# Performance work log

Measured on AMD Instinct MI355X. Metric: run time of the kernel, lower is better.

## Reference

```python
import jax, jax.numpy as jnp
import numpy as np

N = 50000
E = 800000
D = 512
H = 256
K = 16
COLLAPSE_REG = 1.0


def setup_inputs() -> dict:
    key = jax.random.key(0)
    ks = jax.random.split(key, 8)
    embeddings = jax.random.normal(ks[0], (N, D), dtype=jnp.float32)
    edge_src = jax.random.randint(ks[1], (E,), 0, N, dtype=jnp.int32)
    edge_dst = jax.random.randint(ks[2], (E,), 0, N, dtype=jnp.int32)
    # GCNConv params (glorot-ish scaling)
    W1 = jax.random.normal(ks[3], (D, H), dtype=jnp.float32) / np.sqrt(D)
    b1 = jnp.zeros((H,), dtype=jnp.float32)
    W2 = jax.random.normal(ks[4], (H, H), dtype=jnp.float32) / np.sqrt(H)
    b2 = jnp.zeros((H,), dtype=jnp.float32)
    Wa = jax.random.normal(ks[5], (H, K), dtype=jnp.float32) / np.sqrt(H)
    ba = jnp.zeros((K,), dtype=jnp.float32)
    return {"embeddings": embeddings, "edge_src": edge_src, "edge_dst": edge_dst,
            "W1": W1, "b1": b1, "W2": W2, "b2": b2, "Wa": Wa, "ba": ba}


def _gcn_conv(x, W, b, src, dst, dis):
    # PyG GCNConv: transform then D^{-1/2}(A+I)D^{-1/2} aggregation + bias.
    x = x @ W                                   # [N, out]
    norm = dis[src] * dis[dst]                  # [E]
    agg = jax.ops.segment_sum(x[src] * norm[:, None], dst, num_segments=N)
    agg = agg + (dis * dis)[:, None] * x        # self-loop term
    return agg + b


def reference(embeddings, edge_src, edge_dst, W1, b1, W2, b2, Wa, ba):
    # symmetric-norm degrees with self-loops (edge weight 1)
    deg = 1.0 + jax.ops.segment_sum(jnp.ones((E,), jnp.float32), edge_dst, num_segments=N)
    dis = jax.lax.rsqrt(deg)                    # deg > 0 always (self-loop)

    x = jax.nn.selu(_gcn_conv(embeddings, W1, b1, edge_src, edge_dst, dis))
    x_skip = x  # dropout is identity in eval
    x = jax.nn.selu(_gcn_conv(x, W2, b2, edge_src, edge_dst, dis))
    x = x + x_skip
    assignments = jax.nn.softmax(x @ Wa + ba, axis=1)   # [N, K]

    # ---- DMoN losses (faithful to original, incl. scalar normalizer) ----
    degrees = jax.ops.segment_sum(jnp.ones((E,), jnp.float32), edge_src, num_segments=N)  # row sums of A
    m = degrees.sum() / 2.0
    AS = jax.ops.segment_sum(assignments[edge_dst], edge_src, num_segments=N)  # A @ S, [N, K]
    trace_pooled = jnp.sum(assignments * AS)    # trace(S^T A S)
    dS = degrees @ assignments                  # [K]
    normalizer = jnp.dot(dS, dS) / (2.0 * m)    # scalar (as in original code)
    spectral_loss = -(trace_pooled - K * normalizer) / (2.0 * m)

    cluster_sizes = assignments.sum(axis=0)     # [K]
    collapse_loss = jnp.linalg.norm(cluster_sizes) / N * jnp.sqrt(jnp.float32(K)) - 1.0
    entropy = -jnp.sum(assignments * jnp.log(assignments + 1e-8)) / N
    entropy_loss = -0.1 * entropy
    total_loss = spectral_loss + COLLAPSE_REG * collapse_loss + entropy_loss

    pooled = (assignments / (cluster_sizes + 1e-8)).T @ embeddings  # [K, D]
    return (assignments, pooled, spectral_loss, COLLAPSE_REG * collapse_loss, total_loss, entropy_loss)
```

## Files before the change

### kernel.cpp

```cpp
#include <hip/hip_runtime.h>
#include <hip/hip_fp16.h>
#include <math.h>

#define NN 50000
#define EE 800000
#define DD 512
#define HH 256
#define KK 16
#define NB_SCAN 196

typedef _Float16 half8_t __attribute__((ext_vector_type(8)));
typedef float f32x4 __attribute__((ext_vector_type(4)));

__global__ void zero_kernel(int* __restrict__ p, int n) {
    int i = blockIdx.x * blockDim.x + threadIdx.x;
    if (i < n) p[i] = 0;
}

__global__ void count_kernel(const int4* __restrict__ src4, const int4* __restrict__ dst4,
                             int* __restrict__ indeg, int* __restrict__ outdeg) {
    int e = blockIdx.x * blockDim.x + threadIdx.x;
    if (e < EE / 4) {
        int4 s = src4[e], d = dst4[e];
        atomicAdd(&outdeg[s.x], 1); atomicAdd(&outdeg[s.y], 1);
        atomicAdd(&outdeg[s.z], 1); atomicAdd(&outdeg[s.w], 1);
        atomicAdd(&indeg[d.x], 1);  atomicAdd(&indeg[d.y], 1);
        atomicAdd(&indeg[d.z], 1);  atomicAdd(&indeg[d.w], 1);
    }
}

__global__ void scan_p1(const int* __restrict__ in, int* __restrict__ part, int n,
                        const int* __restrict__ outdeg, float* __restrict__ dis,
                        float* __restrict__ degf) {
    __shared__ int tile[256];
    int t = threadIdx.x;
    int i = blockIdx.x * 256 + t;
    int v = (i < n) ? in[i] : 0;
    tile[t] = v;
    if (i < n) {
        dis[i]  = 1.0f / sqrtf(1.0f + (float)v);
        degf[i] = (float)outdeg[i];
    }
    __syncthreads();
    for (int o = 128; o > 0; o >>= 1) {
        if (t < o) tile[t] += tile[t + o];
        __syncthreads();
    }
    if (t == 0) part[blockIdx.x] = tile[0];
}

__global__ void scan_p2(int* __restrict__ part, int nb, int* __restrict__ off_end) {
    __shared__ int tile[256];
    int t = threadIdx.x;
    int v = (t < nb) ? part[t] : 0;
    tile[t] = v;
    __syncthreads();
    for (int o = 1; o < 256; o <<= 1) {
        int x = (t >= o) ? tile[t - o] : 0;
        __syncthreads();
        tile[t] += x;
        __syncthreads();
    }
    if (t < nb) part[t] = tile[t] - v;
    if (t == 255) *off_end = tile[255];
}

__global__ void scan_p3(const int* __restrict__ in, const int* __restrict__ part,
                        int* __restrict__ out, int n) {
    __shared__ int tile[256];
    int t = threadIdx.x;
    int i = blockIdx.x * 256 + t;
    int v = (i < n) ? in[i] : 0;
    tile[t] = v;
    __syncthreads();
    for (int o = 1; o < 256; o <<= 1) {
        int x = (t >= o) ? tile[t - o] : 0;
        __syncthreads();
        tile[t] += x;
        __syncthreads();
    }
    if (i < n) out[i] = part[blockIdx.x] + tile[t] - v;
}

__global__ void scatter_kernel(const int4* __restrict__ src4, const int4* __restrict__ dst4,
                               const int* __restrict__ off, int* __restrict__ cur,
                               const float* __restrict__ dis,
                               int* __restrict__ nbr, __half* __restrict__ wgt) {
    int e = blockIdx.x * blockDim.x + threadIdx.x;
    if (e < EE / 4) {
        int4 s = src4[e], d = dst4[e];
        int p, q;
        p = atomicAdd(&cur[d.x], 1); q = off[d.x] + p;
        nbr[q] = s.x; wgt[q] = __float2half(dis[s.x] * dis[d.x]);
        p = atomicAdd(&cur[d.y], 1); q = off[d.y] + p;
        nbr[q] = s.y; wgt[q] = __float2half(dis[s.y] * dis[d.y]);
        p = atomicAdd(&cur[d.z], 1); q = off[d.z] + p;
        nbr[q] = s.z; wgt[q] = __float2half(dis[s.z] * dis[d.z]);
        p = atomicAdd(&cur[d.w], 1); q = off[d.w] + p;
        nbr[q] = s.w; wgt[q] = __float2half(dis[s.w] * dis[d.w]);
    }
}

__global__ void transpose_w(const float* __restrict__ W1, __half* __restrict__ Wt1,
                            const float* __restrict__ W2, __half* __restrict__ Wt2,
                            const float* __restrict__ Wa, __half* __restrict__ WaT) {
    int i = blockIdx.x * 256 + threadIdx.x;
    if (i < DD * HH) {
        int k = i / HH, n = i % HH;
        Wt1[(size_t)n * DD + k] = __float2half(W1[i]);
    } else if (i < DD * HH + HH * HH) {
        int j = i - DD * HH;
        int k = j / HH, n = j % HH;
        Wt2[(size_t)n * HH + k] = __float2half(W2[j]);
    } else if (i < DD * HH + HH * HH + HH * KK) {
        int j = i - DD * HH - HH * HH;
        int k = j / KK, n = j % KK;
        WaT[n * HH + k] = __float2half(Wa[j]);
    }
}

template <typename TA, int KDIM>
__global__ __launch_bounds__(256) void mfma_gemm(const TA* __restrict__ A,
                                                 const __half* __restrict__ Bt,
                                                 __half* __restrict__ C, int M) {
    constexpr bool F32 = sizeof(TA) == 4;
    constexpr int SROW = F32 ? 36 : 40;
    constexpr int EPG  = F32 ? 4 : 8;
    constexpr int GPR  = 32 / EPG;
    constexpr int RPP  = 256 / GPR;
    constexpr int NP   = 128 / RPP;
    constexpr int KI   = KDIM / 32;

    __shared__ TA As[2][128 * SROW];

    int t = threadIdx.x;
    int wave = t >> 6, lane = t & 63, quad = lane >> 4, l16 = lane & 15;
    int row0 = blockIdx.x * 128, col0 = blockIdx.y * 128;
    int wm = (wave & 1) * 64, wn = (wave >> 1) * 64;
    int srow = t / GPR, sg = t % GPR;

    f32x4 acc[4][4] = {};
    uint4 sreg[NP];
    uint4 bcur[4];

    const __half* brow[4];
#pragma unroll
    for (int ni = 0; ni < 4; ni++)
        brow[ni] = Bt + (size_t)(col0 + wn + ni * 16 + l16) * KDIM + quad * 8;

    auto gloadA = [&](int k0) {
#pragma unroll
        for (int p = 0; p < NP; p++) {
            int gr = row0 + p * RPP + srow;
            if (gr < M)
                sreg[p] = *(const uint4*)(A + (size_t)gr * KDIM + k0 + sg * EPG);
            else
                sreg[p] = make_uint4(0, 0, 0, 0);
        }
    };
    auto sstore = [&](int buf) {
#pragma unroll
        for (int p = 0; p < NP; p++)
            *(uint4*)&As[buf][(p * RPP + srow) * SROW + sg * EPG] = sreg[p];
    };

    gloadA(0);
#pragma unroll
    for (int ni = 0; ni < 4; ni++) bcur[ni] = *(const uint4*)(brow[ni]);
    sstore(0);
    __syncthreads();

#pragma unroll
    for (int i = 0; i < KI; i++) {
        int cur = i & 1;
        uint4 bnext[4];
        if (i + 1 < KI) {
            gloadA((i + 1) * 32);
#pragma unroll
            for (int ni = 0; ni < 4; ni++)
                bnext[ni] = *(const uint4*)(brow[ni] + (i + 1) * 32);
        }

        half8_t af[4];
#pragma unroll
        for (int mi = 0; mi < 4; mi++) {
            int row = wm + mi * 16 + l16;
            if constexpr (F32) {
                const float* pl = (const float*)&As[cur][0] + row * SROW + quad * 8;
                float4 x0 = *(const float4*)pl;
                float4 x1 = *(const float4*)(pl + 4);
                half8_t h;
                h[0] = (_Float16)x0.x; h[1] = (_Float16)x0.y;
                h[2] = (_Float16)x0.z; h[3] = (_Float16)x0.w;
                h[4] = (_Float16)x1.x; h[5] = (_Float16)x1.y;
                h[6] = (_Float16)x1.z; h[7] = (_Float16)x1.w;
                af[mi] = h;
            } else {
                af[mi] = *(const half8_t*)&As[cur][row * SROW + quad * 8];
            }
        }
#pragma unroll
        for (int mi = 0; mi < 4; mi++)
#pragma unroll
            for (int ni = 0; ni < 4; ni++)
                acc[mi][ni] = __builtin_amdgcn_mfma_f32_16x16x32_f16(
                    af[mi], *(half8_t*)&bcur[ni], acc[mi][ni], 0, 0, 0);

        if (i + 1 < KI) {
            sstore(cur ^ 1);
#pragma unroll
            for (int ni = 0; ni < 4; ni++) bcur[ni] = bnext[ni];
        }
        __syncthreads();
    }

#pragma unroll
    for (int mi = 0; mi < 4; mi++) {
#pragma unroll
        for (int r = 0; r < 4; r++) {
            int rr = row0 + wm + mi * 16 + quad * 4 + r;
            if (rr < M) {
#pragma unroll
                for (int ni = 0; ni < 4; ni++) {
                    int c = col0 + wn + ni * 16 + l16;
                    C[((size_t)(c >> 5) * NN + rr) * 32 + (c & 31)] =
                        __float2half(acc[mi][ni][r]);
                }
            }
        }
    }
}

__device__ inline void fma8(float* acc, uint4 raw, float w) {
    const __half2* h = (const __half2*)&raw;
#pragma unroll
    for (int i = 0; i < 4; i++) {
        float2 f = __half22float2(h[i]);
        acc[2 * i]     += w * f.x;
        acc[2 * i + 1] += w * f.y;
    }
}

__global__ __launch_bounds__(256) void agg_selu(const __half* __restrict__ Ts,
                                                const float* __restrict__ dis,
                                                const int* __restrict__ off,
                                                const int* __restrict__ nbr,
                                                const __half* __restrict__ wgt,
                                                const float* __restrict__ bias,
                                                const __half* skip, __half* out) {
    int t = threadIdx.x;
    int s = blockIdx.x & 7;
    int n = (blockIdx.x >> 3) * 64 + (t >> 2);
    if (n >= NN) return;
    int l4 = t & 3;
    int c4 = l4 * 8;
    const __half* Tsl = Ts + (size_t)s * NN * 32;
    float dn = dis[n];

    float acc[8];
#pragma unroll
    for (int i = 0; i < 8; i++) acc[i] = 0.f;
    fma8(acc, *(const uint4*)(Tsl + (size_t)n * 32 + c4), dn * dn);

    int s0 = off[n], s1 = off[n + 1];
    int base = s0;
    for (; base + 8 <= s1; base += 8) {
        int i0 = __builtin_nontemporal_load(&nbr[base + l4]);
        int i1 = __builtin_nontemporal_load(&nbr[base + 4 + l4]);
        unsigned short u0 = __builtin_nontemporal_load((const unsigned short*)&wgt[base + l4]);
        unsigned short u1 = __builtin_nontemporal_load((const unsigned short*)&wgt[base + 4 + l4]);
        __half h0 = *(__half*)&u0, h1 = *(__half*)&u1;
        float w0f = __half2float(h0), w1f = __half2float(h1);
        int id[8]; float ww[8];
#pragma unroll
        for (int j = 0; j < 4; j++) {
            id[j]     = __shfl(i0, j, 4); ww[j]     = __shfl(w0f, j, 4);
            id[4 + j] = __shfl(i1, j, 4); ww[4 + j] = __shfl(w1f, j, 4);
        }
        uint4 r[8];
#pragma unroll
        for (int j = 0; j < 8; j++)
            r[j] = *(const uint4*)(Tsl + (size_t)id[j] * 32 + c4);
#pragma unroll
        for (int j = 0; j < 8; j++) fma8(acc, r[j], ww[j]);
    }
    for (; base < s1; base += 4) {
        int cnt = min(4, s1 - base);
        int iv = 0; float wv = 0.f;
        if (l4 < cnt) {
            iv = __builtin_nontemporal_load(&nbr[base + l4]);
            unsigned short u = __builtin_nontemporal_load((const unsigned short*)&wgt[base + l4]);
            wv = __half2float(*(__half*)&u);
        }
        for (int j = 0; j < cnt; j++) {
            int idx = __shfl(iv, j, 4);
            float w = __shfl(wv, j, 4);
            fma8(acc, *(const uint4*)(Tsl + (size_t)idx * 32 + c4), w);
        }
    }

    const float scale = 1.0507009873554805f;
    const float alpha = 1.6732632423543772f;
    int cg = s * 32 + c4;
    float4 b0 = *(const float4*)(bias + cg);
    float4 b1 = *(const float4*)(bias + cg + 4);
    float bb[8] = {b0.x, b0.y, b0.z, b0.w, b1.x, b1.y, b1.z, b1.w};
    float sk8[8];
#pragma unroll
    for (int i = 0; i < 8; i++) sk8[i] = 0.f;
    if (skip) {
        uint4 raw = *(const uint4*)(skip + (size_t)n * HH + cg);
        const __half2* h = (const __half2*)&raw;
#pragma unroll
        for (int i = 0; i < 4; i++) {
            float2 f = __half22float2(h[i]);
            sk8[2 * i] = f.x; sk8[2 * i + 1] = f.y;
        }
    }
    _Float16 res[8];
#pragma unroll
    for (int i = 0; i < 8; i++) {
        float v = acc[i] + bb[i];
        float r = v > 0.f ? scale * v : scale * alpha * expm1f(v);
        res[i] = (_Float16)(r + sk8[i]);
    }
    *(uint4*)(out + (size_t)n * HH + cg) = *(uint4*)res;
}

__global__ __launch_bounds__(256) void assign_mfma(const __half* __restrict__ Hb,
                                                   const __half* __restrict__ WaT,
                                                   const float* __restrict__ ba,
                                                   const float* __restrict__ degf,
                                                   float* __restrict__ out_assign,
                                                   __half* __restrict__ out_f16,
                                                   float* __restrict__ scal) {
    int t = threadIdx.x;
    int wave = t >> 6, lane = t & 63, quad = lane >> 4, l16 = lane & 15;
    int nb = blockIdx.x * 256 + wave * 64;

    f32x4 acc[4] = {};
    const __half* bp = WaT + l16 * HH + quad * 8;
    const __half* ap[4];
#pragma unroll
    for (int mi = 0; mi < 4; mi++) {
        int r = nb + mi * 16 + l16;
        if (r >= NN) r = NN - 1;
        ap[mi] = Hb + (size_t)r * HH + quad * 8;
    }
#pragma unroll
    for (int s = 0; s < 8; s++) {
        half8_t bf = *(const half8_t*)(bp + s * 32);
#pragma unroll
        for (int mi = 0; mi < 4; mi++) {
            half8_t af = *(const half8_t*)(ap[mi] + s * 32);
            acc[mi] = __builtin_amdgcn_mfma_f32_16x16x32_f16(af, bf, acc[mi], 0, 0, 0);
        }
    }

    float myb = ba[l16];
    float lcs = 0.f, ldS = 0.f, lent = 0.f;
#pragma unroll
    for (int mi = 0; mi < 4; mi++) {
#pragma unroll
        for (int r = 0; r < 4; r++) {
            int node = nb + mi * 16 + quad * 4 + r;
            bool ok = node < NN;
            float logit = acc[mi][r] + myb;
            float mx = logit;
            for (int o = 1; o < 16; o <<= 1) mx = fmaxf(mx, __shfl_xor(mx, o, 16));
            float e = expf(logit - mx);
            float sum = e;
            for (int o = 1; o < 16; o <<= 1) sum += __shfl_xor(sum, o, 16);
            float a = e / sum;
            if (ok) {
                out_assign[(size_t)node * KK + l16] = a;
                out_f16[(size_t)node * KK + l16] = __float2half(a);
                lcs += a;
                ldS += degf[node] * a;
                lent += a * logf(a + 1e-8f);
            }
        }
    }
    lcs += __shfl_xor(lcs, 16); lcs += __shfl_xor(lcs, 32);
    ldS += __shfl_xor(ldS, 16); ldS += __shfl_xor(ldS, 32);
    for (int o = 32; o >= 1; o >>= 1) lent += __shfl_xor(lent, o);
    if (quad == 0) {
        atomicAdd(&scal[l16], lcs);
        atomicAdd(&scal[16 + l16], ldS);
    }
    if (lane == 0) atomicAdd(&scal[33], lent);
}

__device__ inline float dot16h(const __half* a, const __half* b) {
    uint4 a0 = *(const uint4*)a, a1 = *(const uint4*)(a + 8);
    uint4 b0 = *(const uint4*)b, b1 = *(const uint4*)(b + 8);
    float p = 0.f;
    const __half2* xa = (const __half2*)&a0;
    const __half2* xb = (const __half2*)&b0;
#pragma unroll
    for (int i = 0; i < 4; i++) {
        float2 u = __half22float2(xa[i]), v = __half22float2(xb[i]);
        p += u.x * v.x + u.y * v.y;
    }
    xa = (const __half2*)&a1; xb = (const __half2*)&b1;
#pragma unroll
    for (int i = 0; i < 4; i++) {
        float2 u = __half22float2(xa[i]), v = __half22float2(xb[i]);
        p += u.x * v.x + u.y * v.y;
    }
    return p;
}

__global__ __launch_bounds__(256) void edge_trace(const int4* __restrict__ src4,
                                                  const int4* __restrict__ dst4,
                                                  const __half* __restrict__ Ah,
                                                  float* __restrict__ scal) {
    int e = blockIdx.x * blockDim.x + threadIdx.x;
    float p = 0.f;
    if (e < EE / 4) {
        int4 s = src4[e], d = dst4[e];
        p += dot16h(Ah + (size_t)s.x * KK, Ah + (size_t)d.x * KK);
        p += dot16h(Ah + (size_t)s.y * KK, Ah + (size_t)d.y * KK);
        p += dot16h(Ah + (size_t)s.z * KK, Ah + (size_t)d.z * KK);
        p += dot16h(Ah + (size_t)s.w * KK, Ah + (size_t)d.w * KK);
    }
    for (int o = 32; o >= 1; o >>= 1) p += __shfl_xor(p, o);
    __shared__ float sp;
    if (threadIdx.x == 0) sp = 0.f;
    __syncthreads();
    if ((threadIdx.x & 63) == 0) atomicAdd(&sp, p);
    __syncthreads();
    if (threadIdx.x == 0) atomicAdd(&scal[32], sp);
}

#define PCH 125
__global__ __launch_bounds__(256) void pooled_partial(const float* __restrict__ emb,
                                                      const float* __restrict__ assign,
                                                      float* __restrict__ pool_acc) {
    int d = blockIdx.x * 256 + threadIdx.x;
    int c0 = blockIdx.y * PCH;
    float acc[KK];
#pragma unroll
    for (int k = 0; k < KK; k++) acc[k] = 0.f;
    __shared__ float sa[PCH * KK];
    {
        const float4* srcv = (const float4*)(assign + (size_t)c0 * KK);
        float4* dstv = (float4*)sa;
        for (int i = threadIdx.x; i < PCH * KK / 4; i += 256) dstv[i] = srcv[i];
    }
    __syncthreads();
    for (int j = 0; j < PCH; j++) {
        float ev = emb[(size_t)(c0 + j) * DD + d];
#pragma unroll
        for (int k4 = 0; k4 < 4; k4++) {
            float4 s4 = *(const float4*)&sa[j * KK + k4 * 4];
            acc[k4 * 4 + 0] += s4.x * ev;
            acc[k4 * 4 + 1] += s4.y * ev;
            acc[k4 * 4 + 2] += s4.z * ev;
            acc[k4 * 4 + 3] += s4.w * ev;
        }
    }
#pragma unroll
    for (int k = 0; k < KK; k++) atomicAdd(&pool_acc[k * DD + d], acc[k]);
}

__global__ void finalize(const float* __restrict__ pool_acc, const float* __restrict__ scal,
                         float* __restrict__ out) {
    int bx = blockIdx.x, t = threadIdx.x;
    if (bx < 32) {
        int i = bx * 256 + t;
        int k = i / DD;
        out[800000 + i] = pool_acc[i] / (scal[k] + 1e-8f);
    } else if (t == 0) {
        float cs2 = 0.f, ds2 = 0.f;
        for (int k = 0; k < KK; k++) {
            cs2 += scal[k] * scal[k];
            ds2 += scal[16 + k] * scal[16 + k];
        }
        float two_m = (float)EE;
        float normalizer = ds2 / two_m;
        float trace = scal[32];
        float spectral = -(trace - (float)KK * normalizer) / two_m;
        float collapse = sqrtf(cs2) / (float)NN * 4.0f - 1.0f;
        float entl = 0.1f * scal[33] / (float)NN;
        out[808192] = spectral;
        out[808193] = collapse;
        out[808194] = spectral + collapse + entl;
        out[808195] = entl;
    }
}

extern "C" void kernel_launch(void* const* d_in, const int* in_sizes, int n_in,
                              void* d_out, int out_size, void* d_ws, size_t ws_size,
                              hipStream_t stream) {
    const float* emb = (const float*)d_in[0];
    const int* esrc  = (const int*)d_in[1];
    const int* edst  = (const int*)d_in[2];
    const float* W1  = (const float*)d_in[3];
    const float* b1  = (const float*)d_in[4];
    const float* W2  = (const float*)d_in[5];
    const float* b2  = (const float*)d_in[6];
    const float* Wa  = (const float*)d_in[7];
    const float* ba  = (const float*)d_in[8];
    float* out = (float*)d_out;

    int* indeg      = (int*)d_ws;
    int* outdeg     = indeg + 50000;
    int* cur        = outdeg + 50000;
    float* pool_acc = (float*)(cur + 50000);
    float* scal     = pool_acc + 8192;
    int* part       = (int*)(scal + 64);
    int* off        = part + 256;
    int* nbr        = off + 50004;
    float* dis      = (float*)(nbr + 800000);
    float* degf     = dis + 50000;
    __half* wgt     = (__half*)(degf + 50000);
    __half* Wt1     = wgt + 800000;
    __half* Wt2     = Wt1 + 256 * 512;
    __half* WaT     = Wt2 + 256 * 256;
    __half* T       = WaT + 16 * 256;
    __half* Hb      = T + (size_t)NN * HH;
    __half* Ah      = T;

    zero_kernel<<<dim3(619), 256, 0, stream>>>((int*)d_ws, 158256);
    count_kernel<<<dim3(782), 256, 0, stream>>>((const int4*)esrc, (const int4*)edst,
                                                indeg, outdeg);

    scan_p1<<<dim3(NB_SCAN), 256, 0, stream>>>(indeg, part, NN, outdeg, dis, degf);
    scan_p2<<<dim3(1), 256, 0, stream>>>(part, NB_SCAN, off + NN);
    scan_p3<<<dim3(NB_SCAN), 256, 0, stream>>>(indeg, part, off, NN);
    scatter_kernel<<<dim3(782), 256, 0, stream>>>((const int4*)esrc, (const int4*)edst,
                                                  off, cur, dis, nbr, wgt);

    transpose_w<<<dim3(784), 256, 0, stream>>>(W1, Wt1, W2, Wt2, Wa, WaT);

    mfma_gemm<float, DD><<<dim3(392, 2), 256, 0, stream>>>(emb, Wt1, T, NN);
    agg_selu<<<dim3(6256), 256, 0, stream>>>(T, dis, off, nbr, wgt, b1, nullptr, Hb);

    mfma_gemm<__half, HH><<<dim3(392, 2), 256, 0, stream>>>(Hb, Wt2, T, NN);
    agg_selu<<<dim3(6256), 256, 0, stream>>>(T, dis, off, nbr, wgt, b2, Hb, Hb);

    assign_mfma<<<dim3(196), 256, 0, stream>>>(Hb, WaT, ba, degf, out, Ah, scal);
    edge_trace<<<dim3(782), 256, 0, stream>>>((const int4*)esrc, (const int4*)edst, Ah, scal);
    pooled_partial<<<dim3(2, 400), 256, 0, stream>>>(emb, out, pool_acc);
    finalize<<<dim3(33), 256, 0, stream>>>(pool_acc, scal, out);
}
```

Measured before the change: 662.8 us.

## Sort nodes by in-degree for load-balanced aggregation

Builds a counting-sort permutation of nodes by in-degree (histogram, scan, scatter), and the aggregation kernels now process nodes in that order, so threads in a wavefront see similar neighbor counts and diverge less. It adds two small kernels and an extra indirection per node. Output writes become scattered rather than contiguous. Because perm_scatter fills each bin through atomics, the node order within a bin is nondeterministic.

Result: slower. 928.7 us (+40.1%).

```diff
diff --git a/kernel.cpp b/kernel.cpp
--- a/kernel.cpp
+++ b/kernel.cpp
@@ -8,6 +8,8 @@
 #define HH 256
 #define KK 16
 #define NB_SCAN 196
+#define NPAD 50048
+#define NBINS 512
 
 typedef _Float16 half8_t __attribute__((ext_vector_type(8)));
 typedef float f32x4 __attribute__((ext_vector_type(4)));
@@ -31,7 +33,7 @@
 
 __global__ void scan_p1(const int* __restrict__ in, int* __restrict__ part, int n,
                         const int* __restrict__ outdeg, float* __restrict__ dis,
-                        float* __restrict__ degf) {
+                        float* __restrict__ degf, int* __restrict__ hist) {
     __shared__ int tile[256];
     int t = threadIdx.x;
     int i = blockIdx.x * 256 + t;
@@ -40,6 +42,7 @@
     if (i < n) {
         dis[i]  = 1.0f / sqrtf(1.0f + (float)v);
         degf[i] = (float)outdeg[i];
+        atomicAdd(&hist[min(v, NBINS - 1)], 1);
     }
     __syncthreads();
     for (int o = 128; o > 0; o >>= 1) {
@@ -80,6 +83,40 @@
         __syncthreads();
     }
     if (i < n) out[i] = part[blockIdx.x] + tile[t] - v;
+}
+
+__global__ void hist_scan(int* __restrict__ hist, int* __restrict__ perm) {
+    __shared__ int tile[256];
+    __shared__ int carry_s;
+    int t = threadIdx.x;
+    if (t == 0) carry_s = 0;
+    if (t < NPAD - NN) perm[NN + t] = -1;
+    __syncthreads();
+    for (int base = 0; base < NBINS; base += 256) {
+        int v = hist[base + t];
+        tile[t] = v;
+        __syncthreads();
+        for (int o = 1; o < 256; o <<= 1) {
+            int x = (t >= o) ? tile[t - o] : 0;
+            __syncthreads();
+            tile[t] += x;
+            __syncthreads();
+        }
+        hist[base + t] = carry_s + tile[t] - v;
+        __syncthreads();
+        if (t == 0) carry_s += tile[255];
+        __syncthreads();
+    }
+}
+
+__global__ void perm_scatter(const int* __restrict__ indeg, const int* __restrict__ hoff,
+                             int* __restrict__ cursor, int* __restrict__ perm) {
+    int n = blockIdx.x * 256 + threadIdx.x;
+    if (n < NN) {
+        int bin = min(indeg[n], NBINS - 1);
+        int p = atomicAdd(&cursor[bin], 1);
+        perm[hoff[bin] + p] = n;
+    }
 }
 
 __global__ void scatter_kernel(const int4* __restrict__ src4, const int4* __restrict__ dst4,
@@ -246,12 +283,14 @@
                                                 const int* __restrict__ off,
                                                 const int* __restrict__ nbr,
                                                 const __half* __restrict__ wgt,
+                                                const int* __restrict__ perm,
                                                 const float* __restrict__ bias,
                                                 const __half* skip, __half* out) {
     int t = threadIdx.x;
     int s = blockIdx.x & 7;
-    int n = (blockIdx.x >> 3) * 64 + (t >> 2);
-    if (n >= NN) return;
+    int gi = (blockIdx.x >> 3) * 64 + (t >> 2);
+    int n = perm[gi];
+    if (n < 0) return;
     int l4 = t & 3;
     int c4 = l4 * 8;
     const __half* Tsl = Ts + (size_t)s * NN * 32;
@@ -510,8 +549,11 @@
     float* pool_acc = (float*)(cur + 50000);
     float* scal     = pool_acc + 8192;
     int* part       = (int*)(scal + 64);
-    int* off        = part + 256;
-    int* nbr        = off + 50004;
+    int* hist       = part + 256;
+    int* cursor     = hist + 512;
+    int* off        = cursor + 512;
+    int* perm       = off + 50004;
+    int* nbr        = perm + NPAD;
     float* dis      = (float*)(nbr + 800000);
     float* degf     = dis + 50000;
     __half* wgt     = (__half*)(degf + 50000);
@@ -522,23 +564,25 @@
     __half* Hb      = T + (size_t)NN * HH;
     __half* Ah      = T;
 
-    zero_kernel<<<dim3(619), 256, 0, stream>>>((int*)d_ws, 158256);
+    zero_kernel<<<dim3(624), 256, 0, stream>>>((int*)d_ws, 159536);
     count_kernel<<<dim3(782), 256, 0, stream>>>((const int4*)esrc, (const int4*)edst,
                                                 indeg, outdeg);
 
-    scan_p1<<<dim3(NB_SCAN), 256, 0, stream>>>(indeg, part, NN, outdeg, dis, degf);
+    scan_p1<<<dim3(NB_SCAN), 256, 0, stream>>>(indeg, part, NN, outdeg, dis, degf, hist);
     scan_p2<<<dim3(1), 256, 0, stream>>>(part, NB_SCAN, off + NN);
     scan_p3<<<dim3(NB_SCAN), 256, 0, stream>>>(indeg, part, off, NN);
+    hist_scan<<<dim3(1), 256, 0, stream>>>(hist, perm);
+    perm_scatter<<<dim3(NB_SCAN), 256, 0, stream>>>(indeg, hist, cursor, perm);
     scatter_kernel<<<dim3(782), 256, 0, stream>>>((const int4*)esrc, (const int4*)edst,
                                                   off, cur, dis, nbr, wgt);
 
     transpose_w<<<dim3(784), 256, 0, stream>>>(W1, Wt1, W2, Wt2, Wa, WaT);
 
     mfma_gemm<float, DD><<<dim3(392, 2), 256, 0, stream>>>(emb, Wt1, T, NN);
-    agg_selu<<<dim3(6256), 256, 0, stream>>>(T, dis, off, nbr, wgt, b1, nullptr, Hb);
+    agg_selu<<<dim3(6256), 256, 0, stream>>>(T, dis, off, nbr, wgt, perm, b1, nullptr, Hb);
 
     mfma_gemm<__half, HH><<<dim3(392, 2), 256, 0, stream>>>(Hb, Wt2, T, NN);
-    agg_selu<<<dim3(6256), 256, 0, stream>>>(T, dis, off, nbr, wgt, b2, Hb, Hb);
+    agg_selu<<<dim3(6256), 256, 0, stream>>>(T, dis, off, nbr, wgt, perm, b2, Hb, Hb);
 
     assign_mfma<<<dim3(196), 256, 0, stream>>>(Hb, WaT, ba, degf, out, Ah, scal);
     edge_trace<<<dim3(782), 256, 0, stream>>>((const int4*)esrc, (const int4*)edst, Ah, scal);
```
